# Kernel optimization log

Hardware: AMD Instinct MI355X
Metric: run time of the kernel (lower is better)

Reference implementation:

```python
import jax, jax.numpy as jnp
import numpy as np

K = 4096
D = 512
N = 32768

def setup_inputs() -> dict:
    key = jax.random.key(0)
    k1, k2 = jax.random.split(key)
    z_e_x = jax.random.normal(k1, (N, D), dtype=jnp.float32)
    # nn.Embedding initialized uniform(-1/K, 1/K)
    codebook = jax.random.uniform(k2, (K, D), dtype=jnp.float32,
                                  minval=-1.0 / K, maxval=1.0 / K)
    return {"z_e_x": z_e_x, "codebook": codebook}

def reference(z_e_x, codebook):
    # logits[n,k] = <z_e_x[n], codebook[k]>
    logits = jnp.einsum('nd,kd->nk', z_e_x, codebook)
    # softmax is monotone, so argmax(softmax(logits)) == argmax(logits);
    # keep the softmax to mirror the original math (it affects nothing else
    # in the forward output but matches the fusion target exactly).
    y = jax.nn.softmax(logits, axis=1)
    indices = jnp.argmax(y, axis=1)  # [N] int
    return (logits, indices)
```

## Files before the change

kernel.cpp:

```cpp
#include <hip/hip_runtime.h>

#define N_DIM 32768
#define K_DIM 4096
#define D_DIM 512

typedef __attribute__((ext_vector_type(8))) short short8;
typedef __attribute__((ext_vector_type(4))) float f32x4;


__device__ __forceinline__ unsigned short f32_to_bf16_rne(float f) {
  unsigned int u = __builtin_bit_cast(unsigned int, f);
  u += 0x7fffu + ((u >> 16) & 1u);
  return (unsigned short)(u >> 16);
}

__device__ __forceinline__ void gl2lds16(const void* g, void* l) {
  __builtin_amdgcn_global_load_lds(
      (const __attribute__((address_space(1))) unsigned int*)g,
      (__attribute__((address_space(3))) unsigned int*)l, 16, 0, 0);
}


__global__ __launch_bounds__(256) void cvt_bf16(const float* __restrict__ in,
                                                unsigned short* __restrict__ out,
                                                int n4) {
  int i = blockIdx.x * 256 + threadIdx.x;
  if (i < n4) {
    float4 f = ((const float4*)in)[i];
    ushort4 u;
    u.x = f32_to_bf16_rne(f.x);
    u.y = f32_to_bf16_rne(f.y);
    u.z = f32_to_bf16_rne(f.z);
    u.w = f32_to_bf16_rne(f.w);
    ((ushort4*)out)[i] = u;
  }
}


__global__ __launch_bounds__(256) void gemm_bf16(const unsigned short* __restrict__ A,
                                                 const unsigned short* __restrict__ B,
                                                 float* __restrict__ C) {
  __shared__ __align__(16) short As[128 * 32];
  __shared__ __align__(16) short Bs[128 * 32];

  const int tid = threadIdx.x;
  const int l   = tid & 63;
  const int w   = tid >> 6;
  const int wr  = w >> 1;
  const int wc  = w & 1;
  const int m   = l & 15;
  const int q   = l >> 4;

  const int blockCol = blockIdx.x * 128;
  const int blockRow = blockIdx.y * 128;

  const int lrow   = l >> 2;
  const int lchunk = (l & 3) * 8;
  const unsigned short* ga0 = A + (size_t)(blockRow + w * 16 + lrow) * D_DIM + lchunk;
  const unsigned short* ga1 = ga0 + (size_t)64 * D_DIM;
  const unsigned short* gb0 = B + (size_t)(blockCol + w * 16 + lrow) * D_DIM + lchunk;
  const unsigned short* gb1 = gb0 + (size_t)64 * D_DIM;
  short* la0 = As + w * 512;
  short* la1 = As + (w + 4) * 512;
  short* lb0 = Bs + w * 512;
  short* lb1 = Bs + (w + 4) * 512;

  f32x4 acc[4][4] = {};

  for (int k0 = 0; k0 < D_DIM; k0 += 32) {
    gl2lds16(ga0, la0);
    gl2lds16(ga1, la1);
    gl2lds16(gb0, lb0);
    gl2lds16(gb1, lb1);
    __syncthreads();

    short8 af[4], bfr[4];
#pragma unroll
    for (int mi = 0; mi < 4; mi++)
      af[mi] = *(const short8*)(As + (wr * 64 + mi * 16 + m) * 32 + q * 8);
#pragma unroll
    for (int ni = 0; ni < 4; ni++)
      bfr[ni] = *(const short8*)(Bs + (wc * 64 + ni * 16 + m) * 32 + q * 8);

#pragma unroll
    for (int mi = 0; mi < 4; mi++)
#pragma unroll
      for (int ni = 0; ni < 4; ni++)
        acc[mi][ni] = __builtin_amdgcn_mfma_f32_16x16x32_bf16(af[mi], bfr[ni], acc[mi][ni], 0, 0, 0);

    __syncthreads();
    ga0 += 32; ga1 += 32; gb0 += 32; gb1 += 32;
  }

#pragma unroll
  for (int mi = 0; mi < 4; mi++) {
#pragma unroll
    for (int r = 0; r < 4; r++) {
      const int row = blockRow + wr * 64 + mi * 16 + q * 4 + r;
      float* crow = C + (size_t)row * K_DIM + blockCol + wc * 64 + m;
#pragma unroll
      for (int ni = 0; ni < 4; ni++) crow[ni * 16] = acc[mi][ni][r];
    }
  }
}


#define DELTA 6.0e-4f
#define MAXCAND 64

__global__ __launch_bounds__(256) void argmax_refine(const float* __restrict__ logits,
                                                     const float* __restrict__ Z,
                                                     const float* __restrict__ CB,
                                                     float* __restrict__ outIdx) {
  const int row  = blockIdx.x;
  const int t    = threadIdx.x;
  const int lane = t & 63;
  const int w    = t >> 6;

  const float4* lr = (const float4*)(logits + (size_t)row * K_DIM);

  float4 v[4];
  float lmax = -3.0e38f;
#pragma unroll
  for (int i = 0; i < 4; i++) {
    v[i] = lr[t + 256 * i];
    lmax = fmaxf(lmax, fmaxf(fmaxf(v[i].x, v[i].y), fmaxf(v[i].z, v[i].w)));
  }
#pragma unroll
  for (int off = 32; off >= 1; off >>= 1) lmax = fmaxf(lmax, __shfl_xor(lmax, off));

  __shared__ float wm[4];
  if (lane == 0) wm[w] = lmax;
  __syncthreads();
  const float thresh = fmaxf(fmaxf(wm[0], wm[1]), fmaxf(wm[2], wm[3])) - DELTA;

  __shared__ int cand[MAXCAND];
  __shared__ int ccount;
  if (t == 0) ccount = 0;
  __syncthreads();
#pragma unroll
  for (int i = 0; i < 4; i++) {
    const float vv[4] = {v[i].x, v[i].y, v[i].z, v[i].w};
#pragma unroll
    for (int j = 0; j < 4; j++) {
      if (vv[j] >= thresh) {
        int idx = atomicAdd(&ccount, 1);
        if (idx < MAXCAND) cand[idx] = (t + 256 * i) * 4 + j;
      }
    }
  }
  __syncthreads();
  const int nc = min(ccount, MAXCAND);

  __shared__ double cval[MAXCAND];
  const float4* zr4 = (const float4*)(Z + (size_t)row * D_DIM);
  for (int c = w; c < nc; c += 4) {
    const int k = cand[c];
    const float4* br4 = (const float4*)(CB + (size_t)k * D_DIM);
    float4 z0 = zr4[lane], z1 = zr4[lane + 64];
    float4 b0 = br4[lane], b1 = br4[lane + 64];
    double s = (double)z0.x * b0.x + (double)z0.y * b0.y +
               (double)z0.z * b0.z + (double)z0.w * b0.w +
               (double)z1.x * b1.x + (double)z1.y * b1.y +
               (double)z1.z * b1.z + (double)z1.w * b1.w;
#pragma unroll
    for (int off = 32; off >= 1; off >>= 1) s += __shfl_xor(s, off);
    if (lane == 0) cval[c] = s;
  }
  __syncthreads();

  if (t == 0) {
    double best = -1.0e300;
    int    bi   = 0x7fffffff;
    for (int c = 0; c < nc; c++) {
      if (cval[c] > best || (cval[c] == best && cand[c] < bi)) {
        best = cval[c];
        bi   = cand[c];
      }
    }
    outIdx[row] = (float)bi;
  }
}


extern "C" void kernel_launch(void* const* d_in, const int* in_sizes, int n_in,
                              void* d_out, int out_size, void* d_ws, size_t ws_size,
                              hipStream_t stream) {
  const float* Z  = (const float*)d_in[0];
  const float* CB = (const float*)d_in[1];
  float* out = (float*)d_out;

  unsigned short* Abf = (unsigned short*)d_ws;
  unsigned short* Bbf = (unsigned short*)d_ws + (size_t)N_DIM * D_DIM;

  cvt_bf16<<<(N_DIM * D_DIM / 4) / 256, 256, 0, stream>>>(Z, Abf, N_DIM * D_DIM / 4);
  cvt_bf16<<<(K_DIM * D_DIM / 4) / 256, 256, 0, stream>>>(CB, Bbf, K_DIM * D_DIM / 4);

  dim3 grid(K_DIM / 128, N_DIM / 128);
  gemm_bf16<<<grid, 256, 0, stream>>>(Abf, Bbf, out);

  argmax_refine<<<N_DIM, 256, 0, stream>>>(out, Z, CB, out + (size_t)N_DIM * K_DIM);
}
```

Before: 867.4 us.

## Fuse per-tile row max into GEMM epilogue; refine argmax only on candidate tiles

The GEMM epilogue now reduces each 128-column tile's row maximum and writes it to a small per-row partial-max buffer in workspace. The argmax kernel uses one wavefront per row: it reads the 32 partial maxima, picks only the tiles within the threshold, scans just those logits, and recomputes candidates in double precision. This avoids re-reading the full 512 MB logits matrix in the argmax pass. The cost is extra shuffles and an extra barrier in the GEMM epilogue.

Result: faster. 820.4 us (-5.4%).

```diff
diff --git a/kernel.cpp b/kernel.cpp
--- a/kernel.cpp
+++ b/kernel.cpp
@@ -3,6 +3,7 @@
 #define N_DIM 32768
 #define K_DIM 4096
 #define D_DIM 512
+#define NTILE 32
 
 typedef __attribute__((ext_vector_type(8))) short short8;
 typedef __attribute__((ext_vector_type(4))) float f32x4;
@@ -39,9 +40,11 @@
 
 __global__ __launch_bounds__(256) void gemm_bf16(const unsigned short* __restrict__ A,
                                                  const unsigned short* __restrict__ B,
-                                                 float* __restrict__ C) {
+                                                 float* __restrict__ C,
+                                                 float* __restrict__ Pmax) {
   __shared__ __align__(16) short As[128 * 32];
   __shared__ __align__(16) short Bs[128 * 32];
+  __shared__ float sMax[128][2];
 
   const int tid = threadIdx.x;
   const int l   = tid & 63;
@@ -102,84 +105,72 @@
       for (int ni = 0; ni < 4; ni++) crow[ni * 16] = acc[mi][ni][r];
     }
   }
+
+#pragma unroll
+  for (int mi = 0; mi < 4; mi++) {
+#pragma unroll
+    for (int r = 0; r < 4; r++) {
+      float vmax = fmaxf(fmaxf(acc[mi][0][r], acc[mi][1][r]),
+                         fmaxf(acc[mi][2][r], acc[mi][3][r]));
+#pragma unroll
+      for (int off = 8; off >= 1; off >>= 1) vmax = fmaxf(vmax, __shfl_xor(vmax, off));
+      if (m == 0) sMax[wr * 64 + mi * 16 + q * 4 + r][wc] = vmax;
+    }
+  }
+  __syncthreads();
+  if (tid < 128) {
+    float rm = fmaxf(sMax[tid][0], sMax[tid][1]);
+    Pmax[(size_t)(blockRow + tid) * NTILE + blockIdx.x] = rm;
+  }
 }
 
 
 #define DELTA 6.0e-4f
-#define MAXCAND 64
 
-__global__ __launch_bounds__(256) void argmax_refine(const float* __restrict__ logits,
-                                                     const float* __restrict__ Z,
-                                                     const float* __restrict__ CB,
-                                                     float* __restrict__ outIdx) {
-  const int row  = blockIdx.x;
-  const int t    = threadIdx.x;
-  const int lane = t & 63;
-  const int w    = t >> 6;
+__global__ __launch_bounds__(256) void finalize_argmax(const float* __restrict__ Pmax,
+                                                       const float* __restrict__ C,
+                                                       const float* __restrict__ Z,
+                                                       const float* __restrict__ CB,
+                                                       float* __restrict__ outIdx) {
+  const int row  = blockIdx.x * 4 + (threadIdx.x >> 6);
+  const int lane = threadIdx.x & 63;
 
-  const float4* lr = (const float4*)(logits + (size_t)row * K_DIM);
+  float pv = (lane < NTILE) ? Pmax[(size_t)row * NTILE + lane] : -3.0e38f;
+  float gmax = pv;
+#pragma unroll
+  for (int off = 32; off >= 1; off >>= 1) gmax = fmaxf(gmax, __shfl_xor(gmax, off));
+  const float th = gmax - DELTA;
 
-  float4 v[4];
-  float lmax = -3.0e38f;
+  unsigned long long tmask = __ballot(lane < NTILE && pv >= th);
+
+  const float4* zr4 = (const float4*)(Z + (size_t)row * D_DIM);
+  const float4 z0 = zr4[lane], z1 = zr4[lane + 64];
+
+  double best = -1.0e300;
+  int    bi   = 0x7fffffff;
+
+  while (tmask) {
+    const int t = __ffsll(tmask) - 1;
+    tmask &= tmask - 1;
+    const float2 c2 = ((const float2*)(C + (size_t)row * K_DIM + t * 128))[lane];
+    unsigned long long cm0 = __ballot(c2.x >= th);
+    unsigned long long cm1 = __ballot(c2.y >= th);
+    while (cm0 | cm1) {
+      int k;
+      if (cm0) { int b = __ffsll(cm0) - 1; cm0 &= cm0 - 1; k = t * 128 + 2 * b; }
+      else     { int b = __ffsll(cm1) - 1; cm1 &= cm1 - 1; k = t * 128 + 2 * b + 1; }
+      const float4* br4 = (const float4*)(CB + (size_t)k * D_DIM);
+      float4 b0 = br4[lane], b1 = br4[lane + 64];
+      double s = (double)z0.x * b0.x + (double)z0.y * b0.y +
+                 (double)z0.z * b0.z + (double)z0.w * b0.w +
+                 (double)z1.x * b1.x + (double)z1.y * b1.y +
+                 (double)z1.z * b1.z + (double)z1.w * b1.w;
 #pragma unroll
-  for (int i = 0; i < 4; i++) {
-    v[i] = lr[t + 256 * i];
-    lmax = fmaxf(lmax, fmaxf(fmaxf(v[i].x, v[i].y), fmaxf(v[i].z, v[i].w)));
-  }
-#pragma unroll
-  for (int off = 32; off >= 1; off >>= 1) lmax = fmaxf(lmax, __shfl_xor(lmax, off));
-
-  __shared__ float wm[4];
-  if (lane == 0) wm[w] = lmax;
-  __syncthreads();
-  const float thresh = fmaxf(fmaxf(wm[0], wm[1]), fmaxf(wm[2], wm[3])) - DELTA;
-
-  __shared__ int cand[MAXCAND];
-  __shared__ int ccount;
-  if (t == 0) ccount = 0;
-  __syncthreads();
-#pragma unroll
-  for (int i = 0; i < 4; i++) {
-    const float vv[4] = {v[i].x, v[i].y, v[i].z, v[i].w};
-#pragma unroll
-    for (int j = 0; j < 4; j++) {
-      if (vv[j] >= thresh) {
-        int idx = atomicAdd(&ccount, 1);
-        if (idx < MAXCAND) cand[idx] = (t + 256 * i) * 4 + j;
-      }
+      for (int off = 32; off >= 1; off >>= 1) s += __shfl_xor(s, off);
+      if (s > best || (s == best && k < bi)) { best = s; bi = k; }
     }
   }
-  __syncthreads();
-  const int nc = min(ccount, MAXCAND);
-
-  __shared__ double cval[MAXCAND];
-  const float4* zr4 = (const float4*)(Z + (size_t)row * D_DIM);
-  for (int c = w; c < nc; c += 4) {
-    const int k = cand[c];
-    const float4* br4 = (const float4*)(CB + (size_t)k * D_DIM);
-    float4 z0 = zr4[lane], z1 = zr4[lane + 64];
-    float4 b0 = br4[lane], b1 = br4[lane + 64];
-    double s = (double)z0.x * b0.x + (double)z0.y * b0.y +
-               (double)z0.z * b0.z + (double)z0.w * b0.w +
-               (double)z1.x * b1.x + (double)z1.y * b1.y +
-               (double)z1.z * b1.z + (double)z1.w * b1.w;
-#pragma unroll
-    for (int off = 32; off >= 1; off >>= 1) s += __shfl_xor(s, off);
-    if (lane == 0) cval[c] = s;
-  }
-  __syncthreads();
-
-  if (t == 0) {
-    double best = -1.0e300;
-    int    bi   = 0x7fffffff;
-    for (int c = 0; c < nc; c++) {
-      if (cval[c] > best || (cval[c] == best && cand[c] < bi)) {
-        best = cval[c];
-        bi   = cand[c];
-      }
-    }
-    outIdx[row] = (float)bi;
-  }
+  if (lane == 0) outIdx[row] = (float)bi;
 }
 
 
@@ -192,12 +183,14 @@
 
   unsigned short* Abf = (unsigned short*)d_ws;
   unsigned short* Bbf = (unsigned short*)d_ws + (size_t)N_DIM * D_DIM;
+  float* Pmax = (float*)(Bbf + (size_t)K_DIM * D_DIM);
 
   cvt_bf16<<<(N_DIM * D_DIM / 4) / 256, 256, 0, stream>>>(Z, Abf, N_DIM * D_DIM / 4);
   cvt_bf16<<<(K_DIM * D_DIM / 4) / 256, 256, 0, stream>>>(CB, Bbf, K_DIM * D_DIM / 4);
 
   dim3 grid(K_DIM / 128, N_DIM / 128);
-  gemm_bf16<<<grid, 256, 0, stream>>>(Abf, Bbf, out);
+  gemm_bf16<<<grid, 256, 0, stream>>>(Abf, Bbf, out, Pmax);
 
-  argmax_refine<<<N_DIM, 256, 0, stream>>>(out, Z, CB, out + (size_t)N_DIM * K_DIM);
+  finalize_argmax<<<N_DIM / 4, 256, 0, stream>>>(Pmax, out, Z, CB,
+                                                 out + (size_t)N_DIM * K_DIM);
 }
```
